# Optimization experiments

Measured on AMD Instinct MI355X. Metric: run time of the kernel, lower is better.

Reference implementation:

```python
import jax, jax.numpy as jnp
import numpy as np

B, C, N = 2, 256, 4096
H = 8
HD = C // H
SCALE = HD ** -0.5


def setup_inputs() -> dict:
    key = jax.random.key(0)
    ks = jax.random.split(key, 5)
    # xavier_normal for Linear weights: std = sqrt(2/(fan_in+fan_out))
    std_qkv = (2.0 / (C + 3 * C)) ** 0.5
    std_proj = (2.0 / (C + C)) ** 0.5
    return {
        "x": jax.random.normal(ks[0], (B, C, N), dtype=jnp.float32),
        "Wqkv": jax.random.normal(ks[1], (C, 3 * C), dtype=jnp.float32) * std_qkv,
        "bqkv": jnp.zeros((3 * C,), dtype=jnp.float32),
        "Wproj": jax.random.normal(ks[2], (C, C), dtype=jnp.float32) * std_proj,
        "bproj": jnp.zeros((C,), dtype=jnp.float32),
    }


def reference(x, Wqkv, bqkv, Wproj, bproj):
    # x: [B, C, N] -> [B, N, C]
    xt = jnp.transpose(x, (0, 2, 1))
    qkv = xt @ Wqkv + bqkv  # [B, N, 3C]
    q, k, v = jnp.split(qkv, 3, axis=-1)
    # [B, N, C] -> [B, H, N, HD]
    def heads(t):
        return jnp.transpose(t.reshape(B, N, H, HD), (0, 2, 1, 3))
    q, k, v = heads(q), heads(k), heads(v)
    logits = jnp.einsum("bhqd,bhkd->bhqk", q, k) * SCALE  # [B, H, N, N]
    logits = jnp.nan_to_num(logits, nan=0.0, posinf=10000.0, neginf=-10000.0)
    attn = jax.nn.softmax(logits, axis=-1)
    out = jnp.einsum("bhqk,bhkd->bhqd", attn, v)  # [B, H, N, HD]
    out = jnp.transpose(out, (0, 2, 1, 3)).reshape(B, N, C)
    out = out @ Wproj + bproj  # [B, N, C]
    return jnp.transpose(out, (0, 2, 1))  # [B, C, N]
```

## Files before the change

### kernel.cpp

```cpp
#include <hip/hip_runtime.h>
#include <math.h>

#define B_   2
#define C_   256
#define N_   4096
#define H_   8
#define HD_  32
#define TC3  768

typedef __attribute__((ext_vector_type(8))) short bf16x8;
typedef __attribute__((ext_vector_type(4))) float f32x4;
typedef __attribute__((ext_vector_type(4))) unsigned int u32x4;
typedef __attribute__((ext_vector_type(4))) unsigned short u16x4;

__device__ __forceinline__ unsigned short f2bf(float x) {
  union { float f; unsigned int u; } v; v.f = x;
  unsigned int r = v.u + 0x7fffu + ((v.u >> 16) & 1u);
  return (unsigned short)(r >> 16);
}
__device__ __forceinline__ float bf2f(unsigned short h) {
  union { float f; unsigned int u; } v; v.u = ((unsigned int)h) << 16;
  return v.f;
}

__global__ __launch_bounds__(256) void qkv_gemm(const float* __restrict__ x,
                                                const float* __restrict__ W,
                                                const float* __restrict__ bias,
                                                float* __restrict__ qkv) {
  __shared__ float Xs[64][65];
  __shared__ float Wst[64][65];
  const int n0 = blockIdx.x * 64, j0 = blockIdx.y * 64, b = blockIdx.z;
  const int t = threadIdx.x;
  const int tx = t & 15, ty = t >> 4;
  float acc[4][4] = {};
  for (int c0 = 0; c0 < C_; c0 += 64) {
#pragma unroll
    for (int i = 0; i < 16; ++i) {
      int idx = t + 256 * i;
      int kk = idx >> 6, nn = idx & 63;
      Xs[kk][nn]  = x[((size_t)b * C_ + c0 + kk) * N_ + n0 + nn];
      Wst[kk][nn] = W[(size_t)(c0 + kk) * TC3 + j0 + nn];
    }
    __syncthreads();
#pragma unroll
    for (int kk = 0; kk < 64; ++kk) {
      float xv[4], wv[4];
#pragma unroll
      for (int a = 0; a < 4; ++a) xv[a] = Xs[kk][ty + 16 * a];
#pragma unroll
      for (int bb = 0; bb < 4; ++bb) wv[bb] = Wst[kk][tx + 16 * bb];
#pragma unroll
      for (int a = 0; a < 4; ++a)
#pragma unroll
        for (int bb = 0; bb < 4; ++bb) acc[a][bb] += xv[a] * wv[bb];
    }
    __syncthreads();
  }
#pragma unroll
  for (int a = 0; a < 4; ++a) {
    int n = n0 + ty + 16 * a;
#pragma unroll
    for (int bb = 0; bb < 4; ++bb) {
      int j = j0 + tx + 16 * bb;
      qkv[((size_t)b * N_ + n) * TC3 + j] = acc[a][bb] + bias[j];
    }
  }
}

__global__ __launch_bounds__(256) void attn_mfma(const float* __restrict__ qkv,
                                                 float* __restrict__ ao) {
  __shared__ unsigned short Qh[64][32], Ql[64][32];
  __shared__ unsigned short Kh[64][32], Kl[64][32];
  __shared__ unsigned short Vth[32][72], Vtl[32][72];
  __shared__ unsigned int   Pint[4][16][68];

  const int qt = blockIdx.x, h = blockIdx.y, b = blockIdx.z;
  const int t = threadIdx.x;
  const int w = t >> 6, l = t & 63;
  const int l15 = l & 15, l4 = l >> 4;
  const int n0 = qt * 64;
  const float scale = 0.17677669529663687f;

  const int d2 = (t & 15) * 2;
  const int jr = (t >> 4) * 4;

  const float* qbase = qkv + ((size_t)b * N_ + n0) * TC3 + h * HD_;

#pragma unroll
  for (int r = 0; r < 4; ++r) {
    int j = jr + r;
    float2 q2 = *reinterpret_cast<const float2*>(qbase + (size_t)j * TC3 + d2);
    q2.x *= scale; q2.y *= scale;
    unsigned short h0 = f2bf(q2.x), h1 = f2bf(q2.y);
    unsigned short g0 = f2bf(q2.x - bf2f(h0)), g1 = f2bf(q2.y - bf2f(h1));
    *reinterpret_cast<unsigned int*>(&Qh[j][d2]) = (unsigned int)h0 | ((unsigned int)h1 << 16);
    *reinterpret_cast<unsigned int*>(&Ql[j][d2]) = (unsigned int)g0 | ((unsigned int)g1 << 16);
  }
  __syncthreads();

  bf16x8 qa_h = *reinterpret_cast<const bf16x8*>(&Qh[w * 16 + l15][l4 * 8]);
  bf16x8 qa_l = *reinterpret_cast<const bf16x8*>(&Ql[w * 16 + l15][l4 * 8]);

  f32x4 oacc[2] = {};
  float s_part[4] = {};

  const float* kvbase = qkv + (size_t)b * N_ * TC3 + h * HD_;

  for (int kv = 0; kv < 64; ++kv) {
    __syncthreads();
    const float* kb = kvbase + (size_t)(kv * 64) * TC3 + C_;
    const float* vb = kvbase + (size_t)(kv * 64) * TC3 + 2 * C_;
    u16x4 vh0, vh1, vl0, vl1;
#pragma unroll
    for (int r = 0; r < 4; ++r) {
      int j = jr + r;
      float2 k2 = *reinterpret_cast<const float2*>(kb + (size_t)j * TC3 + d2);
      unsigned short h0 = f2bf(k2.x), h1 = f2bf(k2.y);
      unsigned short g0 = f2bf(k2.x - bf2f(h0)), g1 = f2bf(k2.y - bf2f(h1));
      *reinterpret_cast<unsigned int*>(&Kh[j][d2]) = (unsigned int)h0 | ((unsigned int)h1 << 16);
      *reinterpret_cast<unsigned int*>(&Kl[j][d2]) = (unsigned int)g0 | ((unsigned int)g1 << 16);
      float2 v2 = *reinterpret_cast<const float2*>(vb + (size_t)j * TC3 + d2);
      unsigned short a0 = f2bf(v2.x), a1 = f2bf(v2.y);
      vh0[r] = a0; vl0[r] = f2bf(v2.x - bf2f(a0));
      vh1[r] = a1; vl1[r] = f2bf(v2.y - bf2f(a1));
    }
    *reinterpret_cast<u16x4*>(&Vth[d2][jr])     = vh0;
    *reinterpret_cast<u16x4*>(&Vth[d2 + 1][jr]) = vh1;
    *reinterpret_cast<u16x4*>(&Vtl[d2][jr])     = vl0;
    *reinterpret_cast<u16x4*>(&Vtl[d2 + 1][jr]) = vl1;
    __syncthreads();

    f32x4 sacc[4];
#pragma unroll
    for (int kc = 0; kc < 4; ++kc) {
      bf16x8 kb_h = *reinterpret_cast<const bf16x8*>(&Kh[kc * 16 + l15][l4 * 8]);
      bf16x8 kb_l = *reinterpret_cast<const bf16x8*>(&Kl[kc * 16 + l15][l4 * 8]);
      f32x4 a = {};
      a = __builtin_amdgcn_mfma_f32_16x16x32_bf16(qa_h, kb_h, a, 0, 0, 0);
      a = __builtin_amdgcn_mfma_f32_16x16x32_bf16(qa_h, kb_l, a, 0, 0, 0);
      a = __builtin_amdgcn_mfma_f32_16x16x32_bf16(qa_l, kb_h, a, 0, 0, 0);
      sacc[kc] = a;
    }

#pragma unroll
    for (int kc = 0; kc < 4; ++kc)
#pragma unroll
      for (int r = 0; r < 4; ++r) {
        float p = __expf(sacc[kc][r] - 8.0f);
        s_part[r] += p;
        unsigned short ph = f2bf(p);
        unsigned short pl = f2bf(p - bf2f(ph));
        Pint[w][l4 * 4 + r][kc * 16 + l15] = (unsigned int)ph | ((unsigned int)pl << 16);
      }

#pragma unroll
    for (int c = 0; c < 2; ++c) {
      const unsigned int* prow = &Pint[w][l15][c * 32 + l4 * 8];
      u32x4 p0 = *reinterpret_cast<const u32x4*>(prow);
      u32x4 p1 = *reinterpret_cast<const u32x4*>(prow + 4);
      union { unsigned int u[4]; bf16x8 v; } ph_, pl_;
      ph_.u[0] = (p0[0] & 0xffffu) | (p0[1] << 16);
      ph_.u[1] = (p0[2] & 0xffffu) | (p0[3] << 16);
      ph_.u[2] = (p1[0] & 0xffffu) | (p1[1] << 16);
      ph_.u[3] = (p1[2] & 0xffffu) | (p1[3] << 16);
      pl_.u[0] = (p0[0] >> 16) | (p0[1] & 0xffff0000u);
      pl_.u[1] = (p0[2] >> 16) | (p0[3] & 0xffff0000u);
      pl_.u[2] = (p1[0] >> 16) | (p1[1] & 0xffff0000u);
      pl_.u[3] = (p1[2] >> 16) | (p1[3] & 0xffff0000u);
#pragma unroll
      for (int dt = 0; dt < 2; ++dt) {
        bf16x8 vb_h = *reinterpret_cast<const bf16x8*>(&Vth[dt * 16 + l15][c * 32 + l4 * 8]);
        bf16x8 vb_l = *reinterpret_cast<const bf16x8*>(&Vtl[dt * 16 + l15][c * 32 + l4 * 8]);
        oacc[dt] = __builtin_amdgcn_mfma_f32_16x16x32_bf16(ph_.v, vb_h, oacc[dt], 0, 0, 0);
        oacc[dt] = __builtin_amdgcn_mfma_f32_16x16x32_bf16(ph_.v, vb_l, oacc[dt], 0, 0, 0);
        oacc[dt] = __builtin_amdgcn_mfma_f32_16x16x32_bf16(pl_.v, vb_h, oacc[dt], 0, 0, 0);
      }
    }
  }

  float lsum[4];
#pragma unroll
  for (int r = 0; r < 4; ++r) {
    float s = s_part[r];
    s += __shfl_xor(s, 1);
    s += __shfl_xor(s, 2);
    s += __shfl_xor(s, 4);
    s += __shfl_xor(s, 8);
    lsum[r] = s;
  }

  float* aob = ao + ((size_t)b * N_ + n0 + w * 16) * C_ + h * HD_;
#pragma unroll
  for (int dt = 0; dt < 2; ++dt)
#pragma unroll
    for (int r = 0; r < 4; ++r) {
      int q = l4 * 4 + r;
      aob[(size_t)q * C_ + dt * 16 + l15] = oacc[dt][r] / lsum[r];
    }
}

__global__ __launch_bounds__(256) void proj_gemm(const float* __restrict__ ao,
                                                 const float* __restrict__ W,
                                                 const float* __restrict__ bias,
                                                 float* __restrict__ out) {
  __shared__ float Xs[64][65];
  __shared__ float Wst[64][65];
  const int n0 = blockIdx.x * 64, co0 = blockIdx.y * 64, b = blockIdx.z;
  const int t = threadIdx.x;
  const int tx = t & 15, ty = t >> 4;
  float acc[4][4] = {};
  for (int c0 = 0; c0 < C_; c0 += 64) {
#pragma unroll
    for (int i = 0; i < 16; ++i) {
      int idx = t + 256 * i;
      {
        int kk = idx & 63, nn = idx >> 6;
        Xs[kk][nn] = ao[((size_t)b * N_ + n0 + nn) * C_ + c0 + kk];
      }
      {
        int kk = idx >> 6, jj = idx & 63;
        Wst[kk][jj] = W[(size_t)(c0 + kk) * C_ + co0 + jj];
      }
    }
    __syncthreads();
#pragma unroll
    for (int kk = 0; kk < 64; ++kk) {
      float xv[4], wv[4];
#pragma unroll
      for (int a = 0; a < 4; ++a) xv[a] = Xs[kk][tx + 16 * a];
#pragma unroll
      for (int bb = 0; bb < 4; ++bb) wv[bb] = Wst[kk][ty + 16 * bb];
#pragma unroll
      for (int a = 0; a < 4; ++a)
#pragma unroll
        for (int bb = 0; bb < 4; ++bb) acc[a][bb] += xv[a] * wv[bb];
    }
    __syncthreads();
  }
#pragma unroll
  for (int bb = 0; bb < 4; ++bb) {
    int co = co0 + ty + 16 * bb;
    float bv = bias[co];
#pragma unroll
    for (int a = 0; a < 4; ++a) {
      int n = n0 + tx + 16 * a;
      out[((size_t)b * C_ + co) * N_ + n] = acc[a][bb] + bv;
    }
  }
}

extern "C" void kernel_launch(void* const* d_in, const int* in_sizes, int n_in,
                              void* d_out, int out_size, void* d_ws, size_t ws_size,
                              hipStream_t stream) {
  const float* x     = (const float*)d_in[0];
  const float* Wqkv  = (const float*)d_in[1];
  const float* bqkv  = (const float*)d_in[2];
  const float* Wproj = (const float*)d_in[3];
  const float* bproj = (const float*)d_in[4];
  float* out = (float*)d_out;

  float* qkv = (float*)d_ws;
  float* ao  = qkv + (size_t)B_ * N_ * TC3;

  qkv_gemm<<<dim3(N_ / 64, TC3 / 64, B_), 256, 0, stream>>>(x, Wqkv, bqkv, qkv);
  attn_mfma<<<dim3(N_ / 64, H_, B_), 256, 0, stream>>>(qkv, ao);
  proj_gemm<<<dim3(N_ / 64, C_ / 64, B_), 256, 0, stream>>>(ao, Wproj, bproj, out);
}
```

Measured before the change: 424.5 us.

## Emit split-bf16 head-major QKV from GEMM and double query tile in attention

```diff
diff --git a/kernel.cpp b/kernel.cpp
--- a/kernel.cpp
+++ b/kernel.cpp
@@ -26,7 +26,12 @@
 __global__ __launch_bounds__(256) void qkv_gemm(const float* __restrict__ x,
                                                 const float* __restrict__ W,
                                                 const float* __restrict__ bias,
-                                                float* __restrict__ qkv) {
+                                                unsigned short* __restrict__ QhG,
+                                                unsigned short* __restrict__ QlG,
+                                                unsigned short* __restrict__ KhG,
+                                                unsigned short* __restrict__ KlG,
+                                                unsigned short* __restrict__ VhG,
+                                                unsigned short* __restrict__ VlG) {
   __shared__ float Xs[64][65];
   __shared__ float Wst[64][65];
   const int n0 = blockIdx.x * 64, j0 = blockIdx.y * 64, b = blockIdx.z;
@@ -56,147 +61,168 @@
     }
     __syncthreads();
   }
+  const int which = j0 >> 8;
+  unsigned short *ph, *pl;
+  if (which == 0)      { ph = QhG; pl = QlG; }
+  else if (which == 1) { ph = KhG; pl = KlG; }
+  else                 { ph = VhG; pl = VlG; }
 #pragma unroll
   for (int a = 0; a < 4; ++a) {
     int n = n0 + ty + 16 * a;
 #pragma unroll
     for (int bb = 0; bb < 4; ++bb) {
       int j = j0 + tx + 16 * bb;
-      qkv[((size_t)b * N_ + n) * TC3 + j] = acc[a][bb] + bias[j];
-    }
-  }
-}
-
-__global__ __launch_bounds__(256) void attn_mfma(const float* __restrict__ qkv,
-                                                 float* __restrict__ ao) {
-  __shared__ unsigned short Qh[64][32], Ql[64][32];
-  __shared__ unsigned short Kh[64][32], Kl[64][32];
-  __shared__ unsigned short Vth[32][72], Vtl[32][72];
-  __shared__ unsigned int   Pint[4][16][68];
+      float val = acc[a][bb] + bias[j];
+      if (which == 0) val *= 0.17677669529663687f;
+      int sub = j & 255;
+      int hh = sub >> 5, dd = sub & 31;
+      unsigned short hi = f2bf(val);
+      unsigned short lo = f2bf(val - bf2f(hi));
+      size_t idx = ((size_t)(b * H_ + hh) * N_ + n) * HD_ + dd;
+      ph[idx] = hi; pl[idx] = lo;
+    }
+  }
+}
+
+__global__ __launch_bounds__(256) void attn_mfma(
+    const unsigned short* __restrict__ QhG, const unsigned short* __restrict__ QlG,
+    const unsigned short* __restrict__ KhG, const unsigned short* __restrict__ KlG,
+    const unsigned short* __restrict__ VhG, const unsigned short* __restrict__ VlG,
+    float* __restrict__ ao) {
+  __shared__ __align__(16) unsigned short Khs[64][40], Kls[64][40];
+  __shared__ __align__(16) unsigned short Vths[32][72], Vtls[32][72];
+  __shared__ __align__(16) unsigned int   Pint[4][32][68];
 
   const int qt = blockIdx.x, h = blockIdx.y, b = blockIdx.z;
   const int t = threadIdx.x;
   const int w = t >> 6, l = t & 63;
   const int l15 = l & 15, l4 = l >> 4;
-  const int n0 = qt * 64;
-  const float scale = 0.17677669529663687f;
+  const int n0 = qt * 128;
 
   const int d2 = (t & 15) * 2;
-  const int jr = (t >> 4) * 4;
-
-  const float* qbase = qkv + ((size_t)b * N_ + n0) * TC3 + h * HD_;
-
-#pragma unroll
-  for (int r = 0; r < 4; ++r) {
-    int j = jr + r;
-    float2 q2 = *reinterpret_cast<const float2*>(qbase + (size_t)j * TC3 + d2);
-    q2.x *= scale; q2.y *= scale;
-    unsigned short h0 = f2bf(q2.x), h1 = f2bf(q2.y);
-    unsigned short g0 = f2bf(q2.x - bf2f(h0)), g1 = f2bf(q2.y - bf2f(h1));
-    *reinterpret_cast<unsigned int*>(&Qh[j][d2]) = (unsigned int)h0 | ((unsigned int)h1 << 16);
-    *reinterpret_cast<unsigned int*>(&Ql[j][d2]) = (unsigned int)g0 | ((unsigned int)g1 << 16);
-  }
-  __syncthreads();
-
-  bf16x8 qa_h = *reinterpret_cast<const bf16x8*>(&Qh[w * 16 + l15][l4 * 8]);
-  bf16x8 qa_l = *reinterpret_cast<const bf16x8*>(&Ql[w * 16 + l15][l4 * 8]);
-
-  f32x4 oacc[2] = {};
-  float s_part[4] = {};
-
-  const float* kvbase = qkv + (size_t)b * N_ * TC3 + h * HD_;
+  const int tg = t >> 4;
+
+  const size_t base = (size_t)(b * H_ + h) * N_ * HD_;
+
+  bf16x8 qa_h[2], qa_l[2];
+#pragma unroll
+  for (int mt = 0; mt < 2; ++mt) {
+    size_t gi = base + (size_t)(n0 + w * 32 + mt * 16 + l15) * HD_ + l4 * 8;
+    qa_h[mt] = *reinterpret_cast<const bf16x8*>(&QhG[gi]);
+    qa_l[mt] = *reinterpret_cast<const bf16x8*>(&QlG[gi]);
+  }
+
+  f32x4 oacc[2][2] = {};
+  float s_part[2][4] = {};
 
   for (int kv = 0; kv < 64; ++kv) {
     __syncthreads();
-    const float* kb = kvbase + (size_t)(kv * 64) * TC3 + C_;
-    const float* vb = kvbase + (size_t)(kv * 64) * TC3 + 2 * C_;
-    u16x4 vh0, vh1, vl0, vl1;
+    const int jr = tg * 4;
+    u16x4 vh_c0, vh_c1, vl_c0, vl_c1;
 #pragma unroll
     for (int r = 0; r < 4; ++r) {
       int j = jr + r;
-      float2 k2 = *reinterpret_cast<const float2*>(kb + (size_t)j * TC3 + d2);
-      unsigned short h0 = f2bf(k2.x), h1 = f2bf(k2.y);
-      unsigned short g0 = f2bf(k2.x - bf2f(h0)), g1 = f2bf(k2.y - bf2f(h1));
-      *reinterpret_cast<unsigned int*>(&Kh[j][d2]) = (unsigned int)h0 | ((unsigned int)h1 << 16);
-      *reinterpret_cast<unsigned int*>(&Kl[j][d2]) = (unsigned int)g0 | ((unsigned int)g1 << 16);
-      float2 v2 = *reinterpret_cast<const float2*>(vb + (size_t)j * TC3 + d2);
-      unsigned short a0 = f2bf(v2.x), a1 = f2bf(v2.y);
-      vh0[r] = a0; vl0[r] = f2bf(v2.x - bf2f(a0));
-      vh1[r] = a1; vl1[r] = f2bf(v2.y - bf2f(a1));
-    }
-    *reinterpret_cast<u16x4*>(&Vth[d2][jr])     = vh0;
-    *reinterpret_cast<u16x4*>(&Vth[d2 + 1][jr]) = vh1;
-    *reinterpret_cast<u16x4*>(&Vtl[d2][jr])     = vl0;
-    *reinterpret_cast<u16x4*>(&Vtl[d2 + 1][jr]) = vl1;
-    __syncthreads();
-
-    f32x4 sacc[4];
+      size_t gi = base + (size_t)(kv * 64 + j) * HD_ + d2;
+      *reinterpret_cast<unsigned int*>(&Khs[j][d2]) =
+          *reinterpret_cast<const unsigned int*>(&KhG[gi]);
+      *reinterpret_cast<unsigned int*>(&Kls[j][d2]) =
+          *reinterpret_cast<const unsigned int*>(&KlG[gi]);
+      unsigned int vh = *reinterpret_cast<const unsigned int*>(&VhG[gi]);
+      unsigned int vl = *reinterpret_cast<const unsigned int*>(&VlG[gi]);
+      vh_c0[r] = (unsigned short)vh; vh_c1[r] = (unsigned short)(vh >> 16);
+      vl_c0[r] = (unsigned short)vl; vl_c1[r] = (unsigned short)(vl >> 16);
+    }
+    *reinterpret_cast<u16x4*>(&Vths[d2][jr])     = vh_c0;
+    *reinterpret_cast<u16x4*>(&Vths[d2 + 1][jr]) = vh_c1;
+    *reinterpret_cast<u16x4*>(&Vtls[d2][jr])     = vl_c0;
+    *reinterpret_cast<u16x4*>(&Vtls[d2 + 1][jr]) = vl_c1;
+    __syncthreads();
+
+    f32x4 sacc[2][4];
 #pragma unroll
     for (int kc = 0; kc < 4; ++kc) {
-      bf16x8 kb_h = *reinterpret_cast<const bf16x8*>(&Kh[kc * 16 + l15][l4 * 8]);
-      bf16x8 kb_l = *reinterpret_cast<const bf16x8*>(&Kl[kc * 16 + l15][l4 * 8]);
-      f32x4 a = {};
-      a = __builtin_amdgcn_mfma_f32_16x16x32_bf16(qa_h, kb_h, a, 0, 0, 0);
-      a = __builtin_amdgcn_mfma_f32_16x16x32_bf16(qa_h, kb_l, a, 0, 0, 0);
-      a = __builtin_amdgcn_mfma_f32_16x16x32_bf16(qa_l, kb_h, a, 0, 0, 0);
-      sacc[kc] = a;
-    }
-
-#pragma unroll
-    for (int kc = 0; kc < 4; ++kc)
+      bf16x8 kb_h = *reinterpret_cast<const bf16x8*>(&Khs[kc * 16 + l15][l4 * 8]);
+      bf16x8 kb_l = *reinterpret_cast<const bf16x8*>(&Kls[kc * 16 + l15][l4 * 8]);
+#pragma unroll
+      for (int mt = 0; mt < 2; ++mt) {
+        f32x4 a = {};
+        a = __builtin_amdgcn_mfma_f32_16x16x32_bf16(qa_h[mt], kb_h, a, 0, 0, 0);
+        a = __builtin_amdgcn_mfma_f32_16x16x32_bf16(qa_h[mt], kb_l, a, 0, 0, 0);
+        a = __builtin_amdgcn_mfma_f32_16x16x32_bf16(qa_l[mt], kb_h, a, 0, 0, 0);
+        sacc[mt][kc] = a;
+      }
+    }
+
+#pragma unroll
+    for (int mt = 0; mt < 2; ++mt)
+#pragma unroll
+      for (int kc = 0; kc < 4; ++kc)
+#pragma unroll
+        for (int r = 0; r < 4; ++r) {
+          float p = __expf(sacc[mt][kc][r] - 8.0f);
+          s_part[mt][r] += p;
+          unsigned short ph = f2bf(p);
+          unsigned short pl = f2bf(p - bf2f(ph));
+          Pint[w][mt * 16 + l4 * 4 + r][kc * 16 + l15] =
+              (unsigned int)ph | ((unsigned int)pl << 16);
+        }
+    __syncthreads();
+
+#pragma unroll
+    for (int c = 0; c < 2; ++c) {
+      bf16x8 vb_h[2], vb_l[2];
+#pragma unroll
+      for (int dt = 0; dt < 2; ++dt) {
+        vb_h[dt] = *reinterpret_cast<const bf16x8*>(&Vths[dt * 16 + l15][c * 32 + l4 * 8]);
+        vb_l[dt] = *reinterpret_cast<const bf16x8*>(&Vtls[dt * 16 + l15][c * 32 + l4 * 8]);
+      }
+#pragma unroll
+      for (int mt = 0; mt < 2; ++mt) {
+        const unsigned int* prow = &Pint[w][mt * 16 + l15][c * 32 + l4 * 8];
+        u32x4 p0 = *reinterpret_cast<const u32x4*>(prow);
+        u32x4 p1 = *reinterpret_cast<const u32x4*>(prow + 4);
+        union { unsigned int u[4]; bf16x8 v; } ph_, pl_;
+        ph_.u[0] = (p0[0] & 0xffffu) | (p0[1] << 16);
+        ph_.u[1] = (p0[2] & 0xffffu) | (p0[3] << 16);
+        ph_.u[2] = (p1[0] & 0xffffu) | (p1[1] << 16);
+        ph_.u[3] = (p1[2] & 0xffffu) | (p1[3] << 16);
+        pl_.u[0] = (p0[0] >> 16) | (p0[1] & 0xffff0000u);
+        pl_.u[1] = (p0[2] >> 16) | (p0[3] & 0xffff0000u);
+        pl_.u[2] = (p1[0] >> 16) | (p1[1] & 0xffff0000u);
+        pl_.u[3] = (p1[2] >> 16) | (p1[3] & 0xffff0000u);
+#pragma unroll
+        for (int dt = 0; dt < 2; ++dt) {
+          oacc[mt][dt] = __builtin_amdgcn_mfma_f32_16x16x32_bf16(ph_.v, vb_h[dt], oacc[mt][dt], 0, 0, 0);
+          oacc[mt][dt] = __builtin_amdgcn_mfma_f32_16x16x32_bf16(ph_.v, vb_l[dt], oacc[mt][dt], 0, 0, 0);
+          oacc[mt][dt] = __builtin_amdgcn_mfma_f32_16x16x32_bf16(pl_.v, vb_h[dt], oacc[mt][dt], 0, 0, 0);
+        }
+      }
+    }
+  }
+
+  float lsum[2][4];
+#pragma unroll
+  for (int mt = 0; mt < 2; ++mt)
+#pragma unroll
+    for (int r = 0; r < 4; ++r) {
+      float s = s_part[mt][r];
+      s += __shfl_xor(s, 1);
+      s += __shfl_xor(s, 2);
+      s += __shfl_xor(s, 4);
+      s += __shfl_xor(s, 8);
+      lsum[mt][r] = s;
+    }
+
+  float* aob = ao + ((size_t)b * N_ + n0 + w * 32) * C_ + h * HD_;
+#pragma unroll
+  for (int mt = 0; mt < 2; ++mt)
+#pragma unroll
+    for (int dt = 0; dt < 2; ++dt)
 #pragma unroll
       for (int r = 0; r < 4; ++r) {
-        float p = __expf(sacc[kc][r] - 8.0f);
-        s_part[r] += p;
-        unsigned short ph = f2bf(p);
-        unsigned short pl = f2bf(p - bf2f(ph));
-        Pint[w][l4 * 4 + r][kc * 16 + l15] = (unsigned int)ph | ((unsigned int)pl << 16);
-      }
-
-#pragma unroll
-    for (int c = 0; c < 2; ++c) {
-      const unsigned int* prow = &Pint[w][l15][c * 32 + l4 * 8];
-      u32x4 p0 = *reinterpret_cast<const u32x4*>(prow);
-      u32x4 p1 = *reinterpret_cast<const u32x4*>(prow + 4);
-      union { unsigned int u[4]; bf16x8 v; } ph_, pl_;
-      ph_.u[0] = (p0[0] & 0xffffu) | (p0[1] << 16);
-      ph_.u[1] = (p0[2] & 0xffffu) | (p0[3] << 16);
-      ph_.u[2] = (p1[0] & 0xffffu) | (p1[1] << 16);
-      ph_.u[3] = (p1[2] & 0xffffu) | (p1[3] << 16);
-      pl_.u[0] = (p0[0] >> 16) | (p0[1] & 0xffff0000u);
-      pl_.u[1] = (p0[2] >> 16) | (p0[3] & 0xffff0000u);
-      pl_.u[2] = (p1[0] >> 16) | (p1[1] & 0xffff0000u);
-      pl_.u[3] = (p1[2] >> 16) | (p1[3] & 0xffff0000u);
-#pragma unroll
-      for (int dt = 0; dt < 2; ++dt) {
-        bf16x8 vb_h = *reinterpret_cast<const bf16x8*>(&Vth[dt * 16 + l15][c * 32 + l4 * 8]);
-        bf16x8 vb_l = *reinterpret_cast<const bf16x8*>(&Vtl[dt * 16 + l15][c * 32 + l4 * 8]);
-        oacc[dt] = __builtin_amdgcn_mfma_f32_16x16x32_bf16(ph_.v, vb_h, oacc[dt], 0, 0, 0);
-        oacc[dt] = __builtin_amdgcn_mfma_f32_16x16x32_bf16(ph_.v, vb_l, oacc[dt], 0, 0, 0);
-        oacc[dt] = __builtin_amdgcn_mfma_f32_16x16x32_bf16(pl_.v, vb_h, oacc[dt], 0, 0, 0);
-      }
-    }
-  }
-
-  float lsum[4];
-#pragma unroll
-  for (int r = 0; r < 4; ++r) {
-    float s = s_part[r];
-    s += __shfl_xor(s, 1);
-    s += __shfl_xor(s, 2);
-    s += __shfl_xor(s, 4);
-    s += __shfl_xor(s, 8);
-    lsum[r] = s;
-  }
-
-  float* aob = ao + ((size_t)b * N_ + n0 + w * 16) * C_ + h * HD_;
-#pragma unroll
-  for (int dt = 0; dt < 2; ++dt)
-#pragma unroll
-    for (int r = 0; r < 4; ++r) {
-      int q = l4 * 4 + r;
-      aob[(size_t)q * C_ + dt * 16 + l15] = oacc[dt][r] / lsum[r];
-    }
+        int qrow = mt * 16 + l4 * 4 + r;
+        aob[(size_t)qrow * C_ + dt * 16 + l15] = oacc[mt][dt][r] / lsum[mt][r];
+      }
 }
 
 __global__ __launch_bounds__(256) void proj_gemm(const float* __restrict__ ao,
@@ -259,10 +285,18 @@
   const float* bproj = (const float*)d_in[4];
   float* out = (float*)d_out;
 
-  float* qkv = (float*)d_ws;
-  float* ao  = qkv + (size_t)B_ * N_ * TC3;
-
-  qkv_gemm<<<dim3(N_ / 64, TC3 / 64, B_), 256, 0, stream>>>(x, Wqkv, bqkv, qkv);
-  attn_mfma<<<dim3(N_ / 64, H_, B_), 256, 0, stream>>>(qkv, ao);
+  const size_t PS = (size_t)B_ * H_ * N_ * HD_;
+  unsigned short* QhG = (unsigned short*)d_ws;
+  unsigned short* QlG = QhG + PS;
+  unsigned short* KhG = QhG + 2 * PS;
+  unsigned short* KlG = QhG + 3 * PS;
+  unsigned short* VhG = QhG + 4 * PS;
+  unsigned short* VlG = QhG + 5 * PS;
+  float* ao = (float*)(QhG + 6 * PS);
+
+  qkv_gemm<<<dim3(N_ / 64, TC3 / 64, B_), 256, 0, stream>>>(
+      x, Wqkv, bqkv, QhG, QlG, KhG, KlG, VhG, VlG);
+  attn_mfma<<<dim3(N_ / 128, H_, B_), 256, 0, stream>>>(
+      QhG, QlG, KhG, KlG, VhG, VlG, ao);
   proj_gemm<<<dim3(N_ / 64, C_ / 64, B_), 256, 0, stream>>>(ao, Wproj, bproj, out);
 }
```

Measured after the change: 410.2 us. 1.03x faster.
